# Kernel optimization log

Measured on AMD Instinct MI355X. Metric: run time of the kernel, lower is better.

The kernel has to match this reference:

```python
import jax, jax.numpy as jnp
import numpy as np

MIN_NORM = 1e-15
PROJ_EPS = 4e-3


def _artanh(x):
    x = jnp.clip(x, -1 + 1e-7, 1 - 1e-7)
    return 0.5 * (jnp.log1p(x) - jnp.log1p(-x))


def _norm(x):
    return jnp.clip(jnp.linalg.norm(x, axis=-1, keepdims=True), MIN_NORM)


def proj(x, c):
    norm = _norm(x)
    maxnorm = (1.0 - PROJ_EPS) / jnp.sqrt(c)
    return jnp.where(norm > maxnorm, x / norm * maxnorm, x)


def expmap0(u, c):
    sqrt_c = jnp.sqrt(c)
    u_norm = _norm(u)
    return jnp.tanh(sqrt_c * u_norm) * u / (sqrt_c * u_norm)


def logmap0(p, c):
    sqrt_c = jnp.sqrt(c)
    p_norm = _norm(p)
    return _artanh(sqrt_c * p_norm) * p / (sqrt_c * p_norm)


def mobius_add(x, y, c):
    x2 = jnp.sum(x * x, axis=-1, keepdims=True)
    y2 = jnp.sum(y * y, axis=-1, keepdims=True)
    xy = jnp.sum(x * y, axis=-1, keepdims=True)
    num = (1 + 2 * c * xy + c * y2) * x + (1 - c * x2) * y
    denom = 1 + 2 * c * xy + c * c * x2 * y2
    return num / jnp.clip(denom, MIN_NORM)


def mobius_matvec(m, x, c):
    sqrt_c = jnp.sqrt(c)
    x_norm = _norm(x)
    mx = x @ m.T
    mx_norm = _norm(mx)
    res = jnp.tanh(mx_norm / x_norm * _artanh(sqrt_c * x_norm)) * mx / (mx_norm * sqrt_c)
    zero_row = jnp.all(mx == 0, axis=-1, keepdims=True)
    return jnp.where(zero_row, jnp.zeros_like(res), res)


def setup_inputs() -> dict:
    key = jax.random.key(0)
    k1, k2, k3, k4, k5 = jax.random.split(key, 5)
    n, d, e = 50000, 128, 800000
    c = jnp.float32(1.0)
    x = 0.1 * jax.random.normal(k1, (n, d), dtype=jnp.float32)
    x = proj(x, c)  # points on the Poincare ball
    adj = jax.random.randint(k2, (2, e), 0, n, dtype=jnp.int64)
    w = jax.random.uniform(k3, (e,), dtype=jnp.float32)
    weight = jax.random.normal(k4, (d, d), dtype=jnp.float32) * (1.0 / np.sqrt(d))
    bias = jax.random.normal(k5, (d,), dtype=jnp.float32) * 0.01
    return {"x": x, "adj": adj, "w": w, "weight": weight, "bias": bias}


def reference(x, adj, w, weight, bias):
    c_in = jnp.float32(1.0)
    c_out = jnp.float32(1.0)
    n = x.shape[0]

    # HypLinear (dropout p=0 -> identity on weight)
    mv = mobius_matvec(weight, x, c_in)
    res = proj(mv, c_in)
    b = bias.reshape(1, -1)  # proj_tan0 is identity on the Poincare ball
    hyp_bias = proj(expmap0(b, c_in), c_in)
    h = proj(mobius_add(res, hyp_bias, c_in), c_in)

    # HypAgg: logmap0 -> weighted segment_sum over edges -> expmap0 -> proj
    s, r = adj[0], adj[1]
    ht = logmap0(h, c_in)
    x_s = ht[s] * w[:, None]  # [E, d]
    x_agg = jax.ops.segment_sum(x_s, r, num_segments=n)
    h = proj(expmap0(x_agg, c_in), c_in)

    # HypAct: act(logmap0) -> expmap0 -> proj
    xt = jax.nn.relu(logmap0(h, c_in))
    out = proj(expmap0(xt, c_out), c_out)
    return (out, adj)
```

## Files before the change

kernel.cpp:

```cpp
#include <hip/hip_runtime.h>
#include <math.h>

#define MAXN 0.996f
#define MINN 1e-15f
#define CAP  5120
#define CAPQ 1536

typedef __bf16   bf16x8  __attribute__((ext_vector_type(8)));
typedef _Float16 halfx8  __attribute__((ext_vector_type(8)));
typedef _Float16 half2_t __attribute__((ext_vector_type(2)));
typedef float    floatx4 __attribute__((ext_vector_type(4)));

__device__ __forceinline__ float wsum(float v){
  v += __shfl_xor(v, 32);
  v += __shfl_xor(v, 16);
  v += __shfl_xor(v, 8);
  v += __shfl_xor(v, 4);
  v += __shfl_xor(v, 2);
  v += __shfl_xor(v, 1);
  return v;
}

__device__ __forceinline__ float artanh_(float v){
  v = fminf(fmaxf(v, -1.f + 1e-7f), 1.f - 1e-7f);
  return 0.5f * (log1pf(v) - log1pf(-v));
}

__device__ __forceinline__ int block_excl_scan(int v, int tid, int* wsums){
  int lane = tid & 63, wid = tid >> 6;
  int iv = v;
#pragma unroll
  for(int o = 1; o < 64; o <<= 1){
    int t = __shfl_up(iv, o);
    if(lane >= o) iv += t;
  }
  if(lane == 63) wsums[wid] = iv;
  __syncthreads();
  int wbase = 0;
  for(int k = 0; k < wid; k++) wbase += wsums[k];
  return wbase + iv - v;
}

__global__ __launch_bounds__(256)
void fusedA_kernel(const float* __restrict__ x, const float* __restrict__ W,
                   const float* __restrict__ bias, _Float16* __restrict__ ht, int n,
                   const int* __restrict__ adj, const float* __restrict__ w,
                   float* __restrict__ adj_out, int* __restrict__ bucketSize,
                   int2* __restrict__ part, int E, int nA)
{
  __shared__ __align__(16) char smem[43264];
  const int tid = threadIdx.x;

  if(blockIdx.x < nA){
    int* hist  = (int*)smem;
    int* wcur  = (int*)(smem + 4096);
    int* lbase = (int*)(smem + 8192);
    int* gbase = (int*)(smem + 9216);
    int* wsA   = (int*)(smem + 10240);
    int2* stag = (int2*)(smem + 10256);

    const int wv = tid >> 6;
#pragma unroll
    for(int k = 0; k < 4; k++) hist[k*256 + tid] = 0;
    __syncthreads();

    const int e0 = blockIdx.x * 4096;
    int p0r[16], p1r[16];
#pragma unroll
    for(int k = 0; k < 16; k++){
      int e = e0 + k*256 + tid;
      if(e < E){
        int s = adj[e];
        int r = adj[e + E];
        float we = w[e];
        adj_out[e]     = (float)s;
        adj_out[e + E] = (float)r;
        int b = r >> 8;
        p0r[k] = s | ((r & 255) << 16) | (b << 24);
        p1r[k] = __float_as_int(we);
        atomicAdd(&hist[wv*256 + b], 1);
      }
    }
    __syncthreads();
    int h0 = hist[0*256+tid], h1 = hist[1*256+tid], h2 = hist[2*256+tid], h3 = hist[3*256+tid];
    int cb = h0 + h1 + h2 + h3;
    int lb = block_excl_scan(cb, tid, wsA);
    lbase[tid]      = lb;
    wcur[0*256+tid] = lb;
    wcur[1*256+tid] = lb + h0;
    wcur[2*256+tid] = lb + h0 + h1;
    wcur[3*256+tid] = lb + h0 + h1 + h2;
    gbase[tid] = cb ? atomicAdd(&bucketSize[tid], cb) : 0;
    __syncthreads();
#pragma unroll
    for(int k = 0; k < 16; k++){
      int e = e0 + k*256 + tid;
      if(e < E){
        int b = ((unsigned)p0r[k]) >> 24;
        int pos = atomicAdd(&wcur[wv*256 + b], 1);
        stag[pos] = make_int2(p0r[k], p1r[k]);
      }
    }
    __syncthreads();
    int total = (e0 + 4096 <= E) ? 4096 : (E - e0);
    for(int i = tid; i < total; i += 256){
      int2 p = stag[i];
      int b = ((unsigned)p.x) >> 24;
      int loc = gbase[b] + (i - lbase[b]);
      if(loc < CAP) part[(size_t)b * CAP + loc] = p;
    }
    return;
  }

  __bf16* Wh   = (__bf16*)smem;
  float* hb_sh = (float*)(smem + 32768);
  float* y2_sh = (float*)(smem + 33280);

  for(int g = tid; g < 2048; g += 256){
    int nr = g >> 4, k16 = g & 15;
    const float* wp = W + nr * 128 + k16 * 8;
    float4 a = *(const float4*)wp;
    float4 b = *(const float4*)(wp + 4);
    bf16x8 h;
    h[0]=(__bf16)a.x; h[1]=(__bf16)a.y; h[2]=(__bf16)a.z; h[3]=(__bf16)a.w;
    h[4]=(__bf16)b.x; h[5]=(__bf16)b.y; h[6]=(__bf16)b.z; h[7]=(__bf16)b.w;
    *(bf16x8*)&Wh[nr * 128 + ((k16 ^ (nr & 15)) << 3)] = h;
  }
  if(tid < 64){
    int l = tid;
    float b0 = bias[l], b1 = bias[l + 64];
    float bn = fmaxf(sqrtf(wsum(b0*b0 + b1*b1)), MINN);
    float sb = tanhf(bn) / bn;
    float hb0 = sb*b0, hb1 = sb*b1;
    float hnn = fmaxf(sqrtf(wsum(hb0*hb0 + hb1*hb1)), MINN);
    if(hnn > MAXN){ float f = MAXN/hnn; hb0 *= f; hb1 *= f; }
    float y2 = wsum(hb0*hb0 + hb1*hb1);
    hb_sh[l] = hb0; hb_sh[l + 64] = hb1;
    if(l == 0) *y2_sh = y2;
  }
  __syncthreads();

  const int lane = tid & 63;
  const int wid  = tid >> 6;
  const int q    = lane >> 4;
  const int n15  = lane & 15;

  const int M0 = (blockIdx.x - nA) * 64 + wid * 16;
  if(M0 >= n) return;

  float hbv[8];
#pragma unroll
  for(int t = 0; t < 8; t++) hbv[t] = hb_sh[t*16 + n15];
  const float y2 = *y2_sh;

  floatx4 acc[8];
#pragma unroll
  for(int t = 0; t < 8; t++) acc[t] = (floatx4){0.f,0.f,0.f,0.f};

  float x2p = 0.f;
  int m = M0 + n15; if(m > n - 1) m = n - 1;
#pragma unroll
  for(int kk = 0; kk < 4; kk++){
    const float* xp = x + (size_t)m * 128 + kk * 32 + q * 8;
    float4 xa = *(const float4*)xp;
    float4 xb = *(const float4*)(xp + 4);
    x2p += xa.x*xa.x + xa.y*xa.y + xa.z*xa.z + xa.w*xa.w
         + xb.x*xb.x + xb.y*xb.y + xb.z*xb.z + xb.w*xb.w;
    bf16x8 a;
    a[0]=(__bf16)xa.x; a[1]=(__bf16)xa.y; a[2]=(__bf16)xa.z; a[3]=(__bf16)xa.w;
    a[4]=(__bf16)xb.x; a[5]=(__bf16)xb.y; a[6]=(__bf16)xb.z; a[7]=(__bf16)xb.w;
    int k16 = kk * 4 + q;
#pragma unroll
    for(int t = 0; t < 8; t++){
      bf16x8 b = *(bf16x8*)&Wh[(t*16 + n15) * 128 + ((k16 ^ n15) << 3)];
      acc[t] = __builtin_amdgcn_mfma_f32_16x16x32_bf16(a, b, acc[t], 0, 0, 0);
    }
  }
  x2p += __shfl_xor(x2p, 16);
  x2p += __shfl_xor(x2p, 32);

  float mp[4], dp[4];
#pragma unroll
  for(int i = 0; i < 4; i++){
    float mpi = 0.f, dpi = 0.f;
#pragma unroll
    for(int t = 0; t < 8; t++){ float v = acc[t][i]; mpi = fmaf(v, v, mpi); dpi = fmaf(v, hbv[t], dpi); }
    mpi += __shfl_xor(mpi, 1); mpi += __shfl_xor(mpi, 2); mpi += __shfl_xor(mpi, 4); mpi += __shfl_xor(mpi, 8);
    dpi += __shfl_xor(dpi, 1); dpi += __shfl_xor(dpi, 2); dpi += __shfl_xor(dpi, 4); dpi += __shfl_xor(dpi, 8);
    mp[i] = mpi; dp[i] = dpi;
  }

  const int li   = lane & 3;
  const int srcl = (((lane >> 2) << 4) | li) & 63;
  float selmp = li==0 ? mp[0] : li==1 ? mp[1] : li==2 ? mp[2] : mp[3];
  float seldp = li==0 ? dp[0] : li==1 ? dp[1] : li==2 ? dp[2] : dp[3];
  float tmp_mp = __shfl(selmp, srcl);
  float tmp_dp = __shfl(seldp, srcl);
  float mxn = fmaxf(sqrtf(tmp_mp), MINN);
  float xn  = fmaxf(sqrtf(x2p), MINN);
  float tt  = tanhf(mxn / xn * artanh_(xn));
  float s1  = tt / mxn;
  float rn  = fmaxf(tt, MINN);
  if(rn > MAXN) s1 *= MAXN / rn;
  float xy    = s1 * tmp_dp;
  float r2    = s1 * s1 * tmp_mp;
  float alpha = 1.f + 2.f*xy + y2;
  float beta  = 1.f - r2;
  float inv   = 1.f / fmaxf(1.f + 2.f*xy + r2*y2, MINN);
  float as1   = alpha * s1;

  float as1b[4], betab[4], invb[4];
#pragma unroll
  for(int i = 0; i < 4; i++){
    int sl = ((lane >> 4) << 2) | i;
    as1b[i]  = __shfl(as1, sl);
    betab[i] = __shfl(beta, sl);
    invb[i]  = __shfl(inv, sl);
  }

  float uv[4][8];
  float u2[4];
#pragma unroll
  for(int i = 0; i < 4; i++){
    float u2i = 0.f;
#pragma unroll
    for(int t = 0; t < 8; t++){
      float u = (as1b[i] * acc[t][i] + betab[i] * hbv[t]) * invb[i];
      uv[i][t] = u;
      u2i = fmaf(u, u, u2i);
    }
    u2i += __shfl_xor(u2i, 1); u2i += __shfl_xor(u2i, 2); u2i += __shfl_xor(u2i, 4); u2i += __shfl_xor(u2i, 8);
    u2[i] = u2i;
  }

  float selu = li==0 ? u2[0] : li==1 ? u2[1] : li==2 ? u2[2] : u2[3];
  float tu   = __shfl(selu, srcl);
  float un = fmaxf(sqrtf(tu), MINN);
  float sc = 1.f, hn = un;
  if(un > MAXN){ sc = MAXN/un; hn = MAXN; }
  float lt = artanh_(hn) / hn * sc;

#pragma unroll
  for(int i = 0; i < 4; i++){
    int grow = M0 + q * 4 + i;
    float lti = __shfl(lt, ((lane >> 4) << 2) | i);
    if(grow < n){
      halfx8 f;
#pragma unroll
      for(int t = 0; t < 8; t++) f[t] = (_Float16)(lti * uv[i][t]);
      *(halfx8*)(ht + (size_t)grow * 128 + n15 * 8) = f;
    }
  }
}

__global__ __launch_bounds__(1024)
void aggB_kernel(const int* __restrict__ bucketSize, const int2* __restrict__ part,
                 const _Float16* __restrict__ ht, float* __restrict__ out, int n)
{
  __shared__ int2     stag[CAPQ];
  __shared__ unsigned epk_l[CAPQ];
  __shared__ int hist[64];
  __shared__ int rowoff[65];
  __shared__ int cursor[64];
  __shared__ int cnt;
  __shared__ float tr[16][4][132];

  const int tid     = threadIdx.x;
  const int b       = blockIdx.x >> 2;
  const int quarter = blockIdx.x & 3;

  if(tid < 64) hist[tid] = 0;
  if(tid == 0) cnt = 0;
  __syncthreads();

  int size = bucketSize[b]; if(size > CAP) size = CAP;
  const int2* src = part + (size_t)b * CAP;
  for(int i = tid; i < size; i += 1024){
    int2 p = src[i];
    int rlo = (((unsigned)p.x) >> 16) & 255;
    if((rlo >> 6) == quarter){
      int pos = atomicAdd(&cnt, 1);
      if(pos < CAPQ){
        stag[pos] = p;
        atomicAdd(&hist[rlo & 63], 1);
      }
    }
  }
  __syncthreads();
  if(tid < 64){
    int v = hist[tid];
    int iv = v;
#pragma unroll
    for(int o = 1; o < 64; o <<= 1){ int t = __shfl_up(iv, o); if(tid >= o) iv += t; }
    rowoff[tid + 1] = iv;
    cursor[tid]     = iv - v;
    if(tid == 0) rowoff[0] = 0;
  }
  int cntc = cnt; if(cntc > CAPQ) cntc = CAPQ;
  __syncthreads();
  for(int i = tid; i < cntc; i += 1024){
    int2 p = stag[i];
    int rl = (((unsigned)p.x) >> 16) & 63;
    int pos = atomicAdd(&cursor[rl], 1);
    unsigned wh = (unsigned)__builtin_bit_cast(unsigned short,
                    (_Float16)__builtin_bit_cast(float, p.y));
    epk_l[pos] = (unsigned)(p.x & 0xFFFF) | (wh << 16);
  }
  __syncthreads();

  const int g_all = tid >> 4;
  const int i     = tid & 15;
  const int wid   = tid >> 6;
  const int g     = (tid >> 4) & 3;
  const int row   = b * 256 + quarter * 64 + g_all;
  const char* htb = (const char*)ht;
  const int ioff  = i << 4;

  half2_t acc2[4];
#pragma unroll
  for(int k = 0; k < 4; k++) acc2[k] = (half2_t){(_Float16)0.f, (_Float16)0.f};

#define EDGE(pk) { \
    int s_ = (int)((pk) & 0xFFFFu); \
    half2_t w2_ = __builtin_bit_cast(half2_t, __builtin_amdgcn_perm(pk, pk, 0x03020302u)); \
    int4 q_ = *(const int4*)(htb + ((s_ << 8) | ioff)); \
    acc2[0] = __builtin_bit_cast(half2_t, q_.x) * w2_ + acc2[0]; \
    acc2[1] = __builtin_bit_cast(half2_t, q_.y) * w2_ + acc2[1]; \
    acc2[2] = __builtin_bit_cast(half2_t, q_.z) * w2_ + acc2[2]; \
    acc2[3] = __builtin_bit_cast(half2_t, q_.w) * w2_ + acc2[3]; \
  }

  if(row < n){
    int beg = rowoff[g_all];
    int m   = rowoff[g_all + 1] - beg;
    int t = 0;
    for(; t + 1 < m; t += 2){
      unsigned pk0 = epk_l[beg + t];
      unsigned pk1 = epk_l[beg + t + 1];
      EDGE(pk0);
      EDGE(pk1);
    }
    if(t < m){ unsigned pk0 = epk_l[beg + t]; EDGE(pk0); }
  }
#undef EDGE

  float acc[8];
#pragma unroll
  for(int k = 0; k < 4; k++){
    acc[2*k]   = (float)acc2[k][0];
    acc[2*k+1] = (float)acc2[k][1];
  }
  float u2p = 0.f;
#pragma unroll
  for(int k = 0; k < 8; k++) u2p = fmaf(acc[k], acc[k], u2p);
  u2p += __shfl_xor(u2p, 1); u2p += __shfl_xor(u2p, 2);
  u2p += __shfl_xor(u2p, 4); u2p += __shfl_xor(u2p, 8);
  float un = fmaxf(sqrtf(u2p), MINN);
  float te = tanhf(un);
  float se = te / un;
  float gn = fmaxf(te, MINN);
  float hn = gn;
  if(gn > MAXN){ se *= MAXN/gn; hn = MAXN; }
  float la = artanh_(hn) / hn * se;
  float l[8];
  float r2p = 0.f;
#pragma unroll
  for(int k = 0; k < 8; k++){ l[k] = fmaxf(la*acc[k], 0.f); r2p = fmaf(l[k], l[k], r2p); }
  r2p += __shfl_xor(r2p, 1); r2p += __shfl_xor(r2p, 2);
  r2p += __shfl_xor(r2p, 4); r2p += __shfl_xor(r2p, 8);
  float rn = fmaxf(sqrtf(r2p), MINN);
  float t2 = tanhf(rn);
  float s2 = t2 / rn;
  float on = fmaxf(t2, MINN);
  if(on > MAXN) s2 *= MAXN/on;

  if(row < n){
#pragma unroll
    for(int k = 0; k < 8; k++) tr[wid][g][k*16 + i] = s2 * l[k];
    float4 o0 = *(float4*)&tr[wid][g][i*8];
    float4 o1 = *(float4*)&tr[wid][g][i*8 + 4];
    float* orow = out + (size_t)row * 128 + i*8;
    *(float4*)orow       = o0;
    *(float4*)(orow + 4) = o1;
  }
}

extern "C" void kernel_launch(void* const* d_in, const int* in_sizes, int n_in,
                              void* d_out, int out_size, void* d_ws, size_t ws_size,
                              hipStream_t stream)
{
  const float* x    = (const float*)d_in[0];
  const int*   adj  = (const int*)  d_in[1];
  const float* w    = (const float*)d_in[2];
  const float* W    = (const float*)d_in[3];
  const float* bias = (const float*)d_in[4];
  const int n = in_sizes[0] / 128;
  const int E = in_sizes[2];

  float* out     = (float*)d_out;
  float* adj_out = out + (size_t)n * 128;

  char* ws = (char*)d_ws;
  _Float16* ht   = (_Float16*)ws;  ws += (size_t)n * 128 * sizeof(_Float16);
  int2*  part    = (int2*)ws;      ws += (size_t)256 * CAP * sizeof(int2);
  int*   bucketSize = (int*)ws;

  const int nA = (E + 4095) / 4096;
  const int nS = (n + 63) / 64;
  const int nB = (n + 255) / 256;

  hipMemsetAsync(bucketSize, 0, 256 * sizeof(int), stream);
  fusedA_kernel<<<nA + nS, 256, 0, stream>>>(x, W, bias, ht, n,
                                             adj, w, adj_out, bucketSize, part, E, nA);
  aggB_kernel<<<nB * 4, 1024, 0, stream>>>(bucketSize, part, ht, out, n);
}
```

Baseline: 143.6 us.

## Bucket edges into 64-row bins directly to skip per-quarter refiltering

The edge partitioning pass now sorts edges into 1024 bins of 64 destination rows instead of 256 bins of 256 rows. Each aggregation block then reads only its own bin and no longer scans a whole 256-row bucket to filter out its quarter. This removes the four-fold redundant reading of the partition buffer and the global staging copy. The aggregation block shrinks to 512 threads, with each thread handling two rows. In exchange, the histogram in the partition kernel uses a single shared histogram, which raises atomic contention. Bins hold at most 1536 edges, so an unusually dense bin could overflow and drop edges.

```diff
diff --git a/kernel.cpp b/kernel.cpp
--- a/kernel.cpp
+++ b/kernel.cpp
@@ -3,7 +3,6 @@
 
 #define MAXN 0.996f
 #define MINN 1e-15f
-#define CAP  5120
 #define CAPQ 1536
 
 typedef __bf16   bf16x8  __attribute__((ext_vector_type(8)));
@@ -48,18 +47,17 @@
                    float* __restrict__ adj_out, int* __restrict__ bucketSize,
                    int2* __restrict__ part, int E, int nA)
 {
-  __shared__ __align__(16) char smem[43264];
+  __shared__ __align__(16) char smem[49408];
   const int tid = threadIdx.x;
 
   if(blockIdx.x < nA){
     int* hist  = (int*)smem;
-    int* wcur  = (int*)(smem + 4096);
+    int* cur   = (int*)(smem + 4096);
     int* lbase = (int*)(smem + 8192);
-    int* gbase = (int*)(smem + 9216);
-    int* wsA   = (int*)(smem + 10240);
-    int2* stag = (int2*)(smem + 10256);
-
-    const int wv = tid >> 6;
+    int* gbase = (int*)(smem + 12288);
+    int* wsA   = (int*)(smem + 16384);
+    int2* stag = (int2*)(smem + 16400);
+
 #pragma unroll
     for(int k = 0; k < 4; k++) hist[k*256 + tid] = 0;
     __syncthreads();
@@ -75,29 +73,30 @@
         float we = w[e];
         adj_out[e]     = (float)s;
         adj_out[e + E] = (float)r;
-        int b = r >> 8;
-        p0r[k] = s | ((r & 255) << 16) | (b << 24);
+        int bin = r >> 6;
+        p0r[k] = s | ((r & 63) << 16) | (bin << 22);
         p1r[k] = __float_as_int(we);
-        atomicAdd(&hist[wv*256 + b], 1);
+        atomicAdd(&hist[bin], 1);
       }
     }
     __syncthreads();
-    int h0 = hist[0*256+tid], h1 = hist[1*256+tid], h2 = hist[2*256+tid], h3 = hist[3*256+tid];
-    int cb = h0 + h1 + h2 + h3;
+    int c0 = hist[4*tid], c1 = hist[4*tid+1], c2 = hist[4*tid+2], c3 = hist[4*tid+3];
+    int cb = c0 + c1 + c2 + c3;
     int lb = block_excl_scan(cb, tid, wsA);
-    lbase[tid]      = lb;
-    wcur[0*256+tid] = lb;
-    wcur[1*256+tid] = lb + h0;
-    wcur[2*256+tid] = lb + h0 + h1;
-    wcur[3*256+tid] = lb + h0 + h1 + h2;
-    gbase[tid] = cb ? atomicAdd(&bucketSize[tid], cb) : 0;
+    int l0 = lb, l1 = lb + c0, l2 = l1 + c1, l3 = l2 + c2;
+    lbase[4*tid] = l0; lbase[4*tid+1] = l1; lbase[4*tid+2] = l2; lbase[4*tid+3] = l3;
+    cur[4*tid]   = l0; cur[4*tid+1]   = l1; cur[4*tid+2]   = l2; cur[4*tid+3]   = l3;
+    gbase[4*tid]   = c0 ? atomicAdd(&bucketSize[4*tid],   c0) : 0;
+    gbase[4*tid+1] = c1 ? atomicAdd(&bucketSize[4*tid+1], c1) : 0;
+    gbase[4*tid+2] = c2 ? atomicAdd(&bucketSize[4*tid+2], c2) : 0;
+    gbase[4*tid+3] = c3 ? atomicAdd(&bucketSize[4*tid+3], c3) : 0;
     __syncthreads();
 #pragma unroll
     for(int k = 0; k < 16; k++){
       int e = e0 + k*256 + tid;
       if(e < E){
-        int b = ((unsigned)p0r[k]) >> 24;
-        int pos = atomicAdd(&wcur[wv*256 + b], 1);
+        int bin = ((unsigned)p0r[k]) >> 22;
+        int pos = atomicAdd(&cur[bin], 1);
         stag[pos] = make_int2(p0r[k], p1r[k]);
       }
     }
@@ -105,9 +104,9 @@
     int total = (e0 + 4096 <= E) ? 4096 : (E - e0);
     for(int i = tid; i < total; i += 256){
       int2 p = stag[i];
-      int b = ((unsigned)p.x) >> 24;
-      int loc = gbase[b] + (i - lbase[b]);
-      if(loc < CAP) part[(size_t)b * CAP + loc] = p;
+      int bin = ((unsigned)p.x) >> 22;
+      int loc = gbase[bin] + (i - lbase[bin]);
+      if(loc < CAPQ) part[(size_t)bin * CAPQ + loc] = p;
     }
     return;
   }
@@ -253,39 +252,34 @@
   }
 }
 
-__global__ __launch_bounds__(1024)
+__global__ __launch_bounds__(512)
 void aggB_kernel(const int* __restrict__ bucketSize, const int2* __restrict__ part,
                  const _Float16* __restrict__ ht, float* __restrict__ out, int n)
 {
-  __shared__ int2     stag[CAPQ];
   __shared__ unsigned epk_l[CAPQ];
   __shared__ int hist[64];
   __shared__ int rowoff[65];
   __shared__ int cursor[64];
-  __shared__ int cnt;
-  __shared__ float tr[16][4][132];
-
-  const int tid     = threadIdx.x;
-  const int b       = blockIdx.x >> 2;
-  const int quarter = blockIdx.x & 3;
+  __shared__ float tr[8][4][132];
+
+  const int tid = threadIdx.x;
+  const int b   = blockIdx.x;
 
   if(tid < 64) hist[tid] = 0;
-  if(tid == 0) cnt = 0;
-  __syncthreads();
-
-  int size = bucketSize[b]; if(size > CAP) size = CAP;
-  const int2* src = part + (size_t)b * CAP;
-  for(int i = tid; i < size; i += 1024){
-    int2 p = src[i];
-    int rlo = (((unsigned)p.x) >> 16) & 255;
-    if((rlo >> 6) == quarter){
-      int pos = atomicAdd(&cnt, 1);
-      if(pos < CAPQ){
-        stag[pos] = p;
-        atomicAdd(&hist[rlo & 63], 1);
-      }
-    }
-  }
+  __syncthreads();
+
+  int size = bucketSize[b]; if(size > CAPQ) size = CAPQ;
+  const int2* src = part + (size_t)b * CAPQ;
+  int2 e0v, e1v, e2v;
+  const bool v0 = tid < size;
+  const bool v1 = tid + 512 < size;
+  const bool v2 = tid + 1024 < size;
+  if(v0) e0v = src[tid];
+  if(v1) e1v = src[tid + 512];
+  if(v2) e2v = src[tid + 1024];
+  if(v0) atomicAdd(&hist[(((unsigned)e0v.x) >> 16) & 63], 1);
+  if(v1) atomicAdd(&hist[(((unsigned)e1v.x) >> 16) & 63], 1);
+  if(v2) atomicAdd(&hist[(((unsigned)e2v.x) >> 16) & 63], 1);
   __syncthreads();
   if(tid < 64){
     int v = hist[tid];
@@ -296,29 +290,25 @@
     cursor[tid]     = iv - v;
     if(tid == 0) rowoff[0] = 0;
   }
-  int cntc = cnt; if(cntc > CAPQ) cntc = CAPQ;
-  __syncthreads();
-  for(int i = tid; i < cntc; i += 1024){
-    int2 p = stag[i];
-    int rl = (((unsigned)p.x) >> 16) & 63;
-    int pos = atomicAdd(&cursor[rl], 1);
-    unsigned wh = (unsigned)__builtin_bit_cast(unsigned short,
-                    (_Float16)__builtin_bit_cast(float, p.y));
-    epk_l[pos] = (unsigned)(p.x & 0xFFFF) | (wh << 16);
-  }
-  __syncthreads();
-
-  const int g_all = tid >> 4;
-  const int i     = tid & 15;
-  const int wid   = tid >> 6;
-  const int g     = (tid >> 4) & 3;
-  const int row   = b * 256 + quarter * 64 + g_all;
+  __syncthreads();
+#define PUTE(ev) { \
+    int rl = (((unsigned)ev.x) >> 16) & 63; \
+    int p = atomicAdd(&cursor[rl], 1); \
+    unsigned wh = (unsigned)__builtin_bit_cast(unsigned short, \
+                    (_Float16)__builtin_bit_cast(float, ev.y)); \
+    epk_l[p] = (unsigned)(ev.x & 0xFFFF) | (wh << 16); }
+  if(v0) PUTE(e0v);
+  if(v1) PUTE(e1v);
+  if(v2) PUTE(e2v);
+#undef PUTE
+  __syncthreads();
+
+  const int gi   = tid >> 4;
+  const int i    = tid & 15;
+  const int wid  = tid >> 6;
+  const int g    = (tid >> 4) & 3;
   const char* htb = (const char*)ht;
-  const int ioff  = i << 4;
-
-  half2_t acc2[4];
-#pragma unroll
-  for(int k = 0; k < 4; k++) acc2[k] = (half2_t){(_Float16)0.f, (_Float16)0.f};
+  const int ioff = i << 4;
 
 #define EDGE(pk) { \
     int s_ = (int)((pk) & 0xFFFFu); \
@@ -330,59 +320,68 @@
     acc2[3] = __builtin_bit_cast(half2_t, q_.w) * w2_ + acc2[3]; \
   }
 
-  if(row < n){
-    int beg = rowoff[g_all];
-    int m   = rowoff[g_all + 1] - beg;
-    int t = 0;
-    for(; t + 1 < m; t += 2){
-      unsigned pk0 = epk_l[beg + t];
-      unsigned pk1 = epk_l[beg + t + 1];
-      EDGE(pk0);
-      EDGE(pk1);
-    }
-    if(t < m){ unsigned pk0 = epk_l[beg + t]; EDGE(pk0); }
+  for(int rp = 0; rp < 2; rp++){
+    const int lr  = gi + rp * 32;
+    const int row = b * 64 + lr;
+
+    half2_t acc2[4];
+#pragma unroll
+    for(int k = 0; k < 4; k++) acc2[k] = (half2_t){(_Float16)0.f, (_Float16)0.f};
+
+    if(row < n){
+      int beg = rowoff[lr];
+      int m   = rowoff[lr + 1] - beg;
+      int t = 0;
+      for(; t + 1 < m; t += 2){
+        unsigned pk0 = epk_l[beg + t];
+        unsigned pk1 = epk_l[beg + t + 1];
+        EDGE(pk0);
+        EDGE(pk1);
+      }
+      if(t < m){ unsigned pk0 = epk_l[beg + t]; EDGE(pk0); }
+    }
+
+    float acc[8];
+#pragma unroll
+    for(int k = 0; k < 4; k++){
+      acc[2*k]   = (float)acc2[k][0];
+      acc[2*k+1] = (float)acc2[k][1];
+    }
+    float u2p = 0.f;
+#pragma unroll
+    for(int k = 0; k < 8; k++) u2p = fmaf(acc[k], acc[k], u2p);
+    u2p += __shfl_xor(u2p, 1); u2p += __shfl_xor(u2p, 2);
+    u2p += __shfl_xor(u2p, 4); u2p += __shfl_xor(u2p, 8);
+    float un = fmaxf(sqrtf(u2p), MINN);
+    float te = tanhf(un);
+    float se = te / un;
+    float gn = fmaxf(te, MINN);
+    float hn = gn;
+    if(gn > MAXN){ se *= MAXN/gn; hn = MAXN; }
+    float la = artanh_(hn) / hn * se;
+    float l[8];
+    float r2p = 0.f;
+#pragma unroll
+    for(int k = 0; k < 8; k++){ l[k] = fmaxf(la*acc[k], 0.f); r2p = fmaf(l[k], l[k], r2p); }
+    r2p += __shfl_xor(r2p, 1); r2p += __shfl_xor(r2p, 2);
+    r2p += __shfl_xor(r2p, 4); r2p += __shfl_xor(r2p, 8);
+    float rn = fmaxf(sqrtf(r2p), MINN);
+    float t2 = tanhf(rn);
+    float s2 = t2 / rn;
+    float on = fmaxf(t2, MINN);
+    if(on > MAXN) s2 *= MAXN/on;
+
+    if(row < n){
+#pragma unroll
+      for(int k = 0; k < 8; k++) tr[wid][g][k*16 + i] = s2 * l[k];
+      float4 o0 = *(float4*)&tr[wid][g][i*8];
+      float4 o1 = *(float4*)&tr[wid][g][i*8 + 4];
+      float* orow = out + (size_t)row * 128 + i*8;
+      *(float4*)orow       = o0;
+      *(float4*)(orow + 4) = o1;
+    }
   }
 #undef EDGE
-
-  float acc[8];
-#pragma unroll
-  for(int k = 0; k < 4; k++){
-    acc[2*k]   = (float)acc2[k][0];
-    acc[2*k+1] = (float)acc2[k][1];
-  }
-  float u2p = 0.f;
-#pragma unroll
-  for(int k = 0; k < 8; k++) u2p = fmaf(acc[k], acc[k], u2p);
-  u2p += __shfl_xor(u2p, 1); u2p += __shfl_xor(u2p, 2);
-  u2p += __shfl_xor(u2p, 4); u2p += __shfl_xor(u2p, 8);
-  float un = fmaxf(sqrtf(u2p), MINN);
-  float te = tanhf(un);
-  float se = te / un;
-  float gn = fmaxf(te, MINN);
-  float hn = gn;
-  if(gn > MAXN){ se *= MAXN/gn; hn = MAXN; }
-  float la = artanh_(hn) / hn * se;
-  float l[8];
-  float r2p = 0.f;
-#pragma unroll
-  for(int k = 0; k < 8; k++){ l[k] = fmaxf(la*acc[k], 0.f); r2p = fmaf(l[k], l[k], r2p); }
-  r2p += __shfl_xor(r2p, 1); r2p += __shfl_xor(r2p, 2);
-  r2p += __shfl_xor(r2p, 4); r2p += __shfl_xor(r2p, 8);
-  float rn = fmaxf(sqrtf(r2p), MINN);
-  float t2 = tanhf(rn);
-  float s2 = t2 / rn;
-  float on = fmaxf(t2, MINN);
-  if(on > MAXN) s2 *= MAXN/on;
-
-  if(row < n){
-#pragma unroll
-    for(int k = 0; k < 8; k++) tr[wid][g][k*16 + i] = s2 * l[k];
-    float4 o0 = *(float4*)&tr[wid][g][i*8];
-    float4 o1 = *(float4*)&tr[wid][g][i*8 + 4];
-    float* orow = out + (size_t)row * 128 + i*8;
-    *(float4*)orow       = o0;
-    *(float4*)(orow + 4) = o1;
-  }
 }
 
 extern "C" void kernel_launch(void* const* d_in, const int* in_sizes, int n_in,
@@ -402,15 +401,15 @@
 
   char* ws = (char*)d_ws;
   _Float16* ht   = (_Float16*)ws;  ws += (size_t)n * 128 * sizeof(_Float16);
-  int2*  part    = (int2*)ws;      ws += (size_t)256 * CAP * sizeof(int2);
+  int2*  part    = (int2*)ws;      ws += (size_t)1024 * CAPQ * sizeof(int2);
   int*   bucketSize = (int*)ws;
 
   const int nA = (E + 4095) / 4096;
   const int nS = (n + 63) / 64;
-  const int nB = (n + 255) / 256;
-
-  hipMemsetAsync(bucketSize, 0, 256 * sizeof(int), stream);
+  const int nB = (n + 63) / 64;
+
+  hipMemsetAsync(bucketSize, 0, 1024 * sizeof(int), stream);
   fusedA_kernel<<<nA + nS, 256, 0, stream>>>(x, W, bias, ht, n,
                                              adj, w, adj_out, bucketSize, part, E, nA);
-  aggB_kernel<<<nB * 4, 1024, 0, stream>>>(bucketSize, part, ht, out, n);
-}
+  aggB_kernel<<<nB, 512, 0, stream>>>(bucketSize, part, ht, out, n);
+}
```

Result: slower. 151.3 us (+5.4%).
